# Kernel optimization log

Measured on AMD Instinct MI355X. Metric: run time of the kernel, lower is better.

## Reference

```python
import jax, jax.numpy as jnp
import numpy as np

B = 64
A_DIM, T_DIM, V_DIM = 512, 1024, 512
H = 96
O1, O2, O3 = 6, 1, 3
HP1 = H + 1  # 97


def setup_inputs() -> dict:
    key = jax.random.key(0)
    ks = jax.random.split(key, 20)
    s = 0.02
    inp = {
        "audios": jax.random.normal(ks[0], (B, A_DIM), jnp.float32),
        "texts": jax.random.normal(ks[1], (B, T_DIM), jnp.float32),
        "videos": jax.random.normal(ks[2], (B, V_DIM), jnp.float32),
        # MLP encoders: Linear(in, hidden) + ReLU (dropout is identity at eval)
        "Wa": jax.random.normal(ks[3], (A_DIM, H), jnp.float32) * s,
        "ba": jnp.zeros((H,), jnp.float32),
        "Wt": jax.random.normal(ks[4], (T_DIM, H), jnp.float32) * s,
        "bt": jnp.zeros((H,), jnp.float32),
        "Wv": jax.random.normal(ks[5], (V_DIM, H), jnp.float32) * s,
        "bv": jnp.zeros((H,), jnp.float32),
        # post-fusion MLP
        "W1": jax.random.normal(ks[6], (HP1 * HP1 * HP1, H), jnp.float32) * s,
        "b1": jnp.zeros((H,), jnp.float32),
        "W2": jax.random.normal(ks[7], (H, H), jnp.float32) * s,
        "b2": jnp.zeros((H,), jnp.float32),
        # output heads
        "Wo1": jax.random.normal(ks[8], (H, O1), jnp.float32) * s,
        "bo1": jnp.zeros((O1,), jnp.float32),
        "Wo2": jax.random.normal(ks[9], (H, O2), jnp.float32) * s,
        "bo2": jnp.zeros((O2,), jnp.float32),
        "Wo3": jax.random.normal(ks[10], (H, O3), jnp.float32) * s,
        "bo3": jnp.zeros((O3,), jnp.float32),
    }
    return inp


def reference(audios, texts, videos, Wa, ba, Wt, bt, Wv, bv,
              W1, b1, W2, b2, Wo1, bo1, Wo2, bo2, Wo3, bo3):
    # encoders (eval mode: dropout = identity)
    ah = jax.nn.relu(audios @ Wa + ba)   # [B, H]
    th = jax.nn.relu(texts @ Wt + bt)    # [B, H]
    vh = jax.nn.relu(videos @ Wv + bv)   # [B, H]

    one = jnp.ones((ah.shape[0], 1), ah.dtype)
    a1 = jnp.concatenate([one, ah], axis=1)  # [B, H+1]
    v1 = jnp.concatenate([one, vh], axis=1)  # [B, H+1]
    t1 = jnp.concatenate([one, th], axis=1)  # [B, H+1]

    # trilinear outer product: bmm(a1[:, :, None], v1[:, None, :]) -> [B, A, V]
    # then bmm with t1 -> [B, A*V, T]; flatten order is (a, v, t)
    fusion = jnp.einsum('ba,bv,bt->bavt', a1, v1, t1).reshape(a1.shape[0], -1)

    y1 = jax.nn.relu(fusion @ W1 + b1)
    features = jax.nn.relu(y1 @ W2 + b2)

    emos_out = features @ Wo1 + bo1
    vals_out = features @ Wo2 + bo2
    sents_out = features @ Wo3 + bo3
    interloss = jnp.zeros((), jnp.float32)
    return (features, emos_out, vals_out, sents_out, interloss)
```

## Files before the change

### kernel.cpp

```cpp
#include <hip/hip_runtime.h>


typedef unsigned int u32;
typedef short frag8s __attribute__((ext_vector_type(8)));
typedef float f32x4 __attribute__((ext_vector_type(4)));

constexpr int NRUN   = 9409;
constexpr int NGROUP = 2353;
constexpr int RBLK   = 776;
constexpr int NW1    = 912673 * 96;
constexpr int G3     = 512;

constexpr int WS_A1T   = 0;
constexpr int WS_V1T   = WS_A1T + 98 * 64;
constexpr int WS_T1T   = WS_V1T + 98 * 64;
constexpr int WS_Y1SUM = WS_T1T + 98 * 64;

__device__ __forceinline__ u32 bfrne(float x) {
    u32 u = __float_as_uint(x);
    return (u + 0x7FFFu + ((u >> 16) & 1u)) >> 16;
}
__device__ __forceinline__ float bflo(u32 p) { return __uint_as_float(p << 16); }
__device__ __forceinline__ float bfhi(u32 p) { return __uint_as_float(p & 0xFFFF0000u); }

__device__ __forceinline__ void async_cp16(float* lds, const float* g) {
    __builtin_amdgcn_global_load_lds((const __attribute__((address_space(1))) u32*)g,
                                     (__attribute__((address_space(3))) u32*)lds, 16, 0, 0);
}

__global__ __launch_bounds__(256) void k1_enc(const float* __restrict__ audios,
                                              const float* __restrict__ texts,
                                              const float* __restrict__ videos,
                                              const float* __restrict__ Wa, const float* __restrict__ ba,
                                              const float* __restrict__ Wt, const float* __restrict__ bt,
                                              const float* __restrict__ Wv, const float* __restrict__ bv,
                                              float* __restrict__ ws) {
    int wg = blockIdx.x, tid = threadIdx.x;
    int lane = tid & 63, wv = tid >> 6;
    if (wg == 288) {
        if (tid < 64) ws[WS_T1T + 97 * 64 + tid] = 0.0f;
        for (int i = tid; i < 6144; i += 256) ws[WS_Y1SUM + i] = 0.0f;
        return;
    }
    int e = wg / 96, h = wg % 96;
    const float* in; const float* W; float bias; int K; int outbase;
    if (e == 0)      { in = audios; W = Wa; bias = ba[h]; K = 512;  outbase = WS_A1T; }
    else if (e == 1) { in = texts;  W = Wt; bias = bt[h]; K = 1024; outbase = WS_T1T; }
    else             { in = videos; W = Wv; bias = bv[h]; K = 512;  outbase = WS_V1T; }
    int nsweep = K >> 8;
    float4 wreg[4];
    for (int s = 0; s < nsweep; s++) {
        int k0i = s * 256 + lane * 4;
        wreg[s] = make_float4(W[(k0i + 0) * 96 + h], W[(k0i + 1) * 96 + h],
                              W[(k0i + 2) * 96 + h], W[(k0i + 3) * 96 + h]);
    }
    for (int pass = 0; pass < 16; pass++) {
        int b = pass * 4 + wv;
        float acc = 0.f;
        for (int s = 0; s < nsweep; s++) {
            float4 iv = ((const float4*)(in + b * K))[s * 64 + lane];
            acc += iv.x * wreg[s].x + iv.y * wreg[s].y + iv.z * wreg[s].z + iv.w * wreg[s].w;
        }
        for (int off = 32; off; off >>= 1) acc += __shfl_down(acc, off, 64);
        if (lane == 0) {
            float v = acc + bias;
            ws[outbase + (h + 1) * 64 + b] = v > 0.f ? v : 0.f;
        }
    }
    if (h == 0 && tid < 64) ws[outbase + tid] = 1.0f;
}

__global__ __launch_bounds__(256) void k3_main(const float* __restrict__ W1,
                                               float* __restrict__ ws) {
    __shared__ float wtile[4][4 * RBLK];
    __shared__ u32   tpk[64 * 65];
    __shared__ float sl[5][256];

    int tid = threadIdx.x, lane = tid & 63, wv = tid >> 6;
    int id = blockIdx.x;
    int g0, gcount;
    if (id < 305) { g0 = id * 5;                 gcount = 5; }
    else          { g0 = 1525 + (id - 305) * 4;  gcount = 4; }
    const int L = gcount * 13;

    for (int i = tid; i < 4096; i += 256) {
        int b_ = i >> 6, p = i & 63;
        u32 v = 0;
        if (p < 49) {
            float e0 = ws[WS_T1T + (2 * p) * 64 + b_];
            float e1 = ws[WS_T1T + (2 * p + 1) * 64 + b_];
            v = bfrne(e0) | (bfrne(e1) << 16);
        }
        tpk[b_ * 65 + p] = v;
    }
    {
        int q2 = tid >> 6, b_ = tid & 63;
#pragma unroll
        for (int g2 = 0; g2 < 5; g2++) {
            float s = 0.f;
            int run = (g0 + g2) * 4 + q2;
            if (g2 < gcount && run < NRUN) {
                int i = run / 97, j = run % 97;
                s = ws[WS_A1T + i * 64 + b_] * ws[WS_V1T + j * 64 + b_];
            }
            sl[g2][tid] = s;
        }
    }

    auto stage = [&](int g, int t, int buf) {
        int idx0 = (g * 4 + wv) * (97 * 96) + t * (8 * 96) + lane * 4;
        float* ldst = &wtile[buf][wv * RBLK];
#pragma unroll
        for (int c = 0; c < 3; c++) {
            int idx = idx0 + c * 256;
            idx = idx < NW1 - 4 ? idx : NW1 - 4;
            async_cp16(ldst + c * 256, W1 + idx);
        }
    };
    int cs_g = g0, cs_t = 0;
    auto stage_next = [&](int buf) {
        stage(cs_g, cs_t, buf);
        if (++cs_t == 13) { cs_t = 0; ++cs_g; }
    };

    stage_next(0); stage_next(1); stage_next(2);
    asm volatile("s_waitcnt vmcnt(6) lgkmcnt(0)" ::: "memory");
    __builtin_amdgcn_s_barrier();

    f32x4 acc[6];
#pragma unroll
    for (int nt = 0; nt < 6; nt++) acc[nt] = f32x4{0.f, 0.f, 0.f, 0.f};

    int b = (wv << 4) + (lane & 15);
    int q = lane >> 4;

    int gi = 0, t = 0;
    for (int u = 0; u < L; ++u) {
        if (u + 3 < L) stage_next((u + 3) & 3);

        float sv = sl[gi][q * 64 + b];
        int pb = b * 65 + t * 4;
        u32 ap[4];
#pragma unroll
        for (int r = 0; r < 4; r++) {
            u32 tp = tpk[pb + r];
            float fe = sv * bflo(tp), fo = sv * bfhi(tp);
            ap[r] = bfrne(fe) | (bfrne(fo) << 16);
        }
        union { u32 u4[4]; frag8s f; } afr;
        afr.u4[0] = ap[0]; afr.u4[1] = ap[1]; afr.u4[2] = ap[2]; afr.u4[3] = ap[3];

        const float* wt0 = &wtile[u & 3][q * RBLK + (lane & 15)];
#pragma unroll
        for (int nt = 0; nt < 6; nt++) {
            union { u32 u4[4]; frag8s f; } bfr;
#pragma unroll
            for (int r = 0; r < 4; r++) {
                u32 w0 = __float_as_uint(wt0[(2 * r) * 96 + nt * 16]);
                u32 w1 = __float_as_uint(wt0[(2 * r + 1) * 96 + nt * 16]);
                bfr.u4[r] = (w0 >> 16) | (w1 & 0xFFFF0000u);
            }
            acc[nt] = __builtin_amdgcn_mfma_f32_16x16x32_bf16(afr.f, bfr.f, acc[nt], 0, 0, 0);
        }

        if (u + 4 <= L)      asm volatile("s_waitcnt vmcnt(6) lgkmcnt(0)" ::: "memory");
        else if (u + 3 == L) asm volatile("s_waitcnt vmcnt(3) lgkmcnt(0)" ::: "memory");
        else                 asm volatile("s_waitcnt vmcnt(0) lgkmcnt(0)" ::: "memory");
        __builtin_amdgcn_s_barrier();

        if (++t == 13) { t = 0; ++gi; }
    }

    float* ysum = ws + WS_Y1SUM;
#pragma unroll
    for (int nt = 0; nt < 6; nt++) {
#pragma unroll
        for (int r = 0; r < 4; r++) {
            int row = (wv << 4) + ((lane >> 4) << 2) + r;
            int col = nt * 16 + (lane & 15);
            atomicAdd(&ysum[row * 96 + col], acc[nt][r]);
        }
    }
}

__global__ __launch_bounds__(256) void k5_final(const float* __restrict__ b1,
                                                const float* __restrict__ W2, const float* __restrict__ b2,
                                                const float* __restrict__ Wo1, const float* __restrict__ bo1,
                                                const float* __restrict__ Wo2, const float* __restrict__ bo2,
                                                const float* __restrict__ Wo3, const float* __restrict__ bo3,
                                                const float* __restrict__ ws, float* __restrict__ out) {
    __shared__ float yl[8 * 96];
    __shared__ float w2l[96 * 97];
    __shared__ float fl[8 * 96];
    int tid = threadIdx.x;
    int row0 = blockIdx.x * 8;
    for (int i = tid; i < 768; i += 256) {
        int go = row0 * 96 + i;
        float acc = b1[i % 96] + ws[WS_Y1SUM + go];
        yl[i] = acc > 0.f ? acc : 0.f;
    }
    for (int i = tid; i < 9216; i += 256) { int k = i / 96, h = i % 96; w2l[k * 97 + h] = W2[i]; }
    __syncthreads();
    for (int i = tid; i < 768; i += 256) {
        int bb = i / 96, h = i % 96;
        float acc = b2[h];
#pragma unroll 8
        for (int k = 0; k < 96; k++) acc += yl[bb * 96 + k] * w2l[k * 97 + h];
        float f = acc > 0.f ? acc : 0.f;
        fl[i] = f; out[(row0 + bb) * 96 + h] = f;
    }
    __syncthreads();
    if (tid < 80) {
        if (tid < 48) {
            int lr = tid / 6, j = tid % 6;
            float acc = bo1[j];
            for (int k = 0; k < 96; k++) acc += fl[lr * 96 + k] * Wo1[k * 6 + j];
            out[6144 + (row0 + lr) * 6 + j] = acc;
        } else if (tid < 56) {
            int lr = tid - 48;
            float acc = bo2[0];
            for (int k = 0; k < 96; k++) acc += fl[lr * 96 + k] * Wo2[k];
            out[6528 + row0 + lr] = acc;
        } else {
            int t2 = tid - 56; int lr = t2 / 3, j = t2 % 3;
            float acc = bo3[j];
            for (int k = 0; k < 96; k++) acc += fl[lr * 96 + k] * Wo3[k * 3 + j];
            out[6592 + (row0 + lr) * 3 + j] = acc;
        }
    }
    if (blockIdx.x == 0 && tid == 0) out[6784] = 0.0f;
}

extern "C" void kernel_launch(void* const* d_in, const int* in_sizes, int n_in,
                              void* d_out, int out_size, void* d_ws, size_t ws_size,
                              hipStream_t stream) {
    (void)in_sizes; (void)n_in; (void)out_size; (void)ws_size;
    const float* audios = (const float*)d_in[0];
    const float* texts  = (const float*)d_in[1];
    const float* videos = (const float*)d_in[2];
    const float* Wa  = (const float*)d_in[3];
    const float* ba  = (const float*)d_in[4];
    const float* Wt  = (const float*)d_in[5];
    const float* bt  = (const float*)d_in[6];
    const float* Wv  = (const float*)d_in[7];
    const float* bv  = (const float*)d_in[8];
    const float* W1  = (const float*)d_in[9];
    const float* b1  = (const float*)d_in[10];
    const float* W2  = (const float*)d_in[11];
    const float* b2  = (const float*)d_in[12];
    const float* Wo1 = (const float*)d_in[13];
    const float* bo1 = (const float*)d_in[14];
    const float* Wo2 = (const float*)d_in[15];
    const float* bo2 = (const float*)d_in[16];
    const float* Wo3 = (const float*)d_in[17];
    const float* bo3 = (const float*)d_in[18];
    float* ws = (float*)d_ws;
    float* outp = (float*)d_out;

    k1_enc<<<289, 256, 0, stream>>>(audios, texts, videos, Wa, ba, Wt, bt, Wv, bv, ws);
    k3_main<<<G3, 256, 0, stream>>>(W1, ws);
    k5_final<<<8, 256, 0, stream>>>(b1, W2, b2, Wo1, bo1, Wo2, bo2, Wo3, bo3, ws, outp);
}
```

Measured before the change: 565.5 us.

## Replace atomic split-K reduction with per-block partials reduced in final kernel

```diff
diff --git a/kernel.cpp b/kernel.cpp
--- a/kernel.cpp
+++ b/kernel.cpp
@@ -11,10 +11,10 @@
 constexpr int NW1    = 912673 * 96;
 constexpr int G3     = 512;
 
-constexpr int WS_A1T   = 0;
-constexpr int WS_V1T   = WS_A1T + 98 * 64;
-constexpr int WS_T1T   = WS_V1T + 98 * 64;
-constexpr int WS_Y1SUM = WS_T1T + 98 * 64;
+constexpr int WS_A1T  = 0;
+constexpr int WS_V1T  = WS_A1T + 98 * 64;
+constexpr int WS_T1T  = WS_V1T + 98 * 64;
+constexpr int WS_PART = WS_T1T + 98 * 64;
 
 __device__ __forceinline__ u32 bfrne(float x) {
     u32 u = __float_as_uint(x);
@@ -39,7 +39,6 @@
     int lane = tid & 63, wv = tid >> 6;
     if (wg == 288) {
         if (tid < 64) ws[WS_T1T + 97 * 64 + tid] = 0.0f;
-        for (int i = tid; i < 6144; i += 256) ws[WS_Y1SUM + i] = 0.0f;
         return;
     }
     int e = wg / 96, h = wg % 96;
@@ -171,64 +170,73 @@
         if (++t == 13) { t = 0; ++gi; }
     }
 
-    float* ysum = ws + WS_Y1SUM;
+    float* part = ws + WS_PART + (size_t)id * 6144;
 #pragma unroll
     for (int nt = 0; nt < 6; nt++) {
 #pragma unroll
         for (int r = 0; r < 4; r++) {
             int row = (wv << 4) + ((lane >> 4) << 2) + r;
             int col = nt * 16 + (lane & 15);
-            atomicAdd(&ysum[row * 96 + col], acc[nt][r]);
-        }
-    }
-}
-
-__global__ __launch_bounds__(256) void k5_final(const float* __restrict__ b1,
+            part[row * 96 + col] = acc[nt][r];
+        }
+    }
+}
+
+__global__ __launch_bounds__(384) void k5_final(const float* __restrict__ b1,
                                                 const float* __restrict__ W2, const float* __restrict__ b2,
                                                 const float* __restrict__ Wo1, const float* __restrict__ bo1,
                                                 const float* __restrict__ Wo2, const float* __restrict__ bo2,
                                                 const float* __restrict__ Wo3, const float* __restrict__ bo3,
                                                 const float* __restrict__ ws, float* __restrict__ out) {
-    __shared__ float yl[8 * 96];
+    __shared__ float red[4][96];
+    __shared__ float yl[96];
     __shared__ float w2l[96 * 97];
-    __shared__ float fl[8 * 96];
+    __shared__ float fl[96];
     int tid = threadIdx.x;
-    int row0 = blockIdx.x * 8;
-    for (int i = tid; i < 768; i += 256) {
-        int go = row0 * 96 + i;
-        float acc = b1[i % 96] + ws[WS_Y1SUM + go];
-        yl[i] = acc > 0.f ? acc : 0.f;
-    }
-    for (int i = tid; i < 9216; i += 256) { int k = i / 96, h = i % 96; w2l[k * 97 + h] = W2[i]; }
+    int row = blockIdx.x;
+    int s = tid / 96;
+    int c = tid - s * 96;
+
+    for (int i = tid; i < 9216; i += 384) { int k = i / 96, h = i % 96; w2l[k * 97 + h] = W2[i]; }
+
+    {
+        float acc = 0.f;
+        const float* p = ws + WS_PART + (size_t)(s * 128) * 6144 + row * 96 + c;
+#pragma unroll 8
+        for (int w = 0; w < 128; w++) acc += p[(size_t)w * 6144];
+        red[s][c] = acc;
+    }
     __syncthreads();
-    for (int i = tid; i < 768; i += 256) {
-        int bb = i / 96, h = i % 96;
-        float acc = b2[h];
+    if (tid < 96) {
+        float y = red[0][tid] + red[1][tid] + red[2][tid] + red[3][tid] + b1[tid];
+        yl[tid] = y > 0.f ? y : 0.f;
+    }
+    __syncthreads();
+    if (tid < 96) {
+        float acc = b2[tid];
 #pragma unroll 8
-        for (int k = 0; k < 96; k++) acc += yl[bb * 96 + k] * w2l[k * 97 + h];
+        for (int k = 0; k < 96; k++) acc += yl[k] * w2l[k * 97 + tid];
         float f = acc > 0.f ? acc : 0.f;
-        fl[i] = f; out[(row0 + bb) * 96 + h] = f;
+        fl[tid] = f; out[row * 96 + tid] = f;
     }
     __syncthreads();
-    if (tid < 80) {
-        if (tid < 48) {
-            int lr = tid / 6, j = tid % 6;
-            float acc = bo1[j];
-            for (int k = 0; k < 96; k++) acc += fl[lr * 96 + k] * Wo1[k * 6 + j];
-            out[6144 + (row0 + lr) * 6 + j] = acc;
-        } else if (tid < 56) {
-            int lr = tid - 48;
+    if (tid < 10) {
+        if (tid < 6) {
+            float acc = bo1[tid];
+            for (int k = 0; k < 96; k++) acc += fl[k] * Wo1[k * 6 + tid];
+            out[6144 + row * 6 + tid] = acc;
+        } else if (tid == 6) {
             float acc = bo2[0];
-            for (int k = 0; k < 96; k++) acc += fl[lr * 96 + k] * Wo2[k];
-            out[6528 + row0 + lr] = acc;
+            for (int k = 0; k < 96; k++) acc += fl[k] * Wo2[k];
+            out[6528 + row] = acc;
         } else {
-            int t2 = tid - 56; int lr = t2 / 3, j = t2 % 3;
+            int j = tid - 7;
             float acc = bo3[j];
-            for (int k = 0; k < 96; k++) acc += fl[lr * 96 + k] * Wo3[k * 3 + j];
-            out[6592 + (row0 + lr) * 3 + j] = acc;
-        }
-    }
-    if (blockIdx.x == 0 && tid == 0) out[6784] = 0.0f;
+            for (int k = 0; k < 96; k++) acc += fl[k] * Wo3[k * 3 + j];
+            out[6592 + row * 3 + j] = acc;
+        }
+    }
+    if (row == 0 && tid == 0) out[6784] = 0.0f;
 }
 
 extern "C" void kernel_launch(void* const* d_in, const int* in_sizes, int n_in,
@@ -259,5 +267,5 @@
 
     k1_enc<<<289, 256, 0, stream>>>(audios, texts, videos, Wa, ba, Wt, bt, Wv, bv, ws);
     k3_main<<<G3, 256, 0, stream>>>(W1, ws);
-    k5_final<<<8, 256, 0, stream>>>(b1, W2, b2, Wo1, bo1, Wo2, bo2, Wo3, bo3, ws, outp);
-}
+    k5_final<<<64, 384, 0, stream>>>(b1, W2, b2, Wo1, bo1, Wo2, bo2, Wo3, bo3, ws, outp);
+}
```

Result: slower. 580.4 us (+2.6%).

## Transpose W1 tile into swizzled LDS layout via 4-byte async loads for vectorized B-fragment reads

Applied to the files above, without the earlier changes.

```diff
diff --git a/kernel.cpp b/kernel.cpp
--- a/kernel.cpp
+++ b/kernel.cpp
@@ -6,8 +6,6 @@
 typedef float f32x4 __attribute__((ext_vector_type(4)));
 
 constexpr int NRUN   = 9409;
-constexpr int NGROUP = 2353;
-constexpr int RBLK   = 776;
 constexpr int NW1    = 912673 * 96;
 constexpr int G3     = 512;
 
@@ -23,9 +21,9 @@
 __device__ __forceinline__ float bflo(u32 p) { return __uint_as_float(p << 16); }
 __device__ __forceinline__ float bfhi(u32 p) { return __uint_as_float(p & 0xFFFF0000u); }
 
-__device__ __forceinline__ void async_cp16(float* lds, const float* g) {
+__device__ __forceinline__ void async_cp4(float* lds, const float* g) {
     __builtin_amdgcn_global_load_lds((const __attribute__((address_space(1))) u32*)g,
-                                     (__attribute__((address_space(3))) u32*)lds, 16, 0, 0);
+                                     (__attribute__((address_space(3))) u32*)lds, 4, 0, 0);
 }
 
 __global__ __launch_bounds__(256) void k1_enc(const float* __restrict__ audios,
@@ -72,7 +70,7 @@
 
 __global__ __launch_bounds__(256) void k3_main(const float* __restrict__ W1,
                                                float* __restrict__ ws) {
-    __shared__ float wtile[4][4 * RBLK];
+    __shared__ float wtile[4][4 * 768];
     __shared__ u32   tpk[64 * 65];
     __shared__ float sl[5][256];
 
@@ -107,14 +105,23 @@
         }
     }
 
+    int goff[12];
+#pragma unroll
+    for (int c = 0; c < 12; c++) {
+        int S = c * 64 + lane;
+        int col = S >> 3;
+        int j = (S & 7) ^ (((S >> 5) & 1) << 2);
+        goff[c] = j * 96 + col;
+    }
+
     auto stage = [&](int g, int t, int buf) {
-        int idx0 = (g * 4 + wv) * (97 * 96) + t * (8 * 96) + lane * 4;
-        float* ldst = &wtile[buf][wv * RBLK];
-#pragma unroll
-        for (int c = 0; c < 3; c++) {
-            int idx = idx0 + c * 256;
-            idx = idx < NW1 - 4 ? idx : NW1 - 4;
-            async_cp16(ldst + c * 256, W1 + idx);
+        int runbase = (g * 4 + wv) * (97 * 96) + t * (8 * 96);
+        float* ldst = &wtile[buf][wv * 768];
+#pragma unroll
+        for (int c = 0; c < 12; c++) {
+            int idx = runbase + goff[c];
+            idx = idx < NW1 - 1 ? idx : NW1 - 1;
+            async_cp4(ldst + c * 64, W1 + idx);
         }
     };
     int cs_g = g0, cs_t = 0;
@@ -124,15 +131,19 @@
     };
 
     stage_next(0); stage_next(1); stage_next(2);
-    asm volatile("s_waitcnt vmcnt(6) lgkmcnt(0)" ::: "memory");
+    asm volatile("s_waitcnt vmcnt(24) lgkmcnt(0)" ::: "memory");
     __builtin_amdgcn_s_barrier();
 
     f32x4 acc[6];
 #pragma unroll
     for (int nt = 0; nt < 6; nt++) acc[nt] = f32x4{0.f, 0.f, 0.f, 0.f};
 
-    int b = (wv << 4) + (lane & 15);
+    int c16 = lane & 15;
+    int b = (wv << 4) + c16;
     int q = lane >> 4;
+    int f = (c16 >> 2) & 1;
+    int blo = q * 768 + c16 * 8 + 4 * f;
+    int bhi = q * 768 + c16 * 8 + 4 * (1 - f);
 
     int gi = 0, t = 0;
     for (int u = 0; u < L; ++u) {
@@ -147,24 +158,24 @@
             float fe = sv * bflo(tp), fo = sv * bfhi(tp);
             ap[r] = bfrne(fe) | (bfrne(fo) << 16);
         }
-        union { u32 u4[4]; frag8s f; } afr;
+        union { u32 u4[4]; frag8s f8; } afr;
         afr.u4[0] = ap[0]; afr.u4[1] = ap[1]; afr.u4[2] = ap[2]; afr.u4[3] = ap[3];
 
-        const float* wt0 = &wtile[u & 3][q * RBLK + (lane & 15)];
+        const float* wb = wtile[u & 3];
 #pragma unroll
         for (int nt = 0; nt < 6; nt++) {
-            union { u32 u4[4]; frag8s f; } bfr;
-#pragma unroll
-            for (int r = 0; r < 4; r++) {
-                u32 w0 = __float_as_uint(wt0[(2 * r) * 96 + nt * 16]);
-                u32 w1 = __float_as_uint(wt0[(2 * r + 1) * 96 + nt * 16]);
-                bfr.u4[r] = (w0 >> 16) | (w1 & 0xFFFF0000u);
-            }
-            acc[nt] = __builtin_amdgcn_mfma_f32_16x16x32_bf16(afr.f, bfr.f, acc[nt], 0, 0, 0);
-        }
-
-        if (u + 4 <= L)      asm volatile("s_waitcnt vmcnt(6) lgkmcnt(0)" ::: "memory");
-        else if (u + 3 == L) asm volatile("s_waitcnt vmcnt(3) lgkmcnt(0)" ::: "memory");
+            f32x4 lo = *(const f32x4*)(wb + blo + nt * 128);
+            f32x4 hi = *(const f32x4*)(wb + bhi + nt * 128);
+            union { u32 u4[4]; frag8s f8; } bfr;
+            bfr.u4[0] = __builtin_amdgcn_perm(__float_as_uint(lo[1]), __float_as_uint(lo[0]), 0x07060302u);
+            bfr.u4[1] = __builtin_amdgcn_perm(__float_as_uint(lo[3]), __float_as_uint(lo[2]), 0x07060302u);
+            bfr.u4[2] = __builtin_amdgcn_perm(__float_as_uint(hi[1]), __float_as_uint(hi[0]), 0x07060302u);
+            bfr.u4[3] = __builtin_amdgcn_perm(__float_as_uint(hi[3]), __float_as_uint(hi[2]), 0x07060302u);
+            acc[nt] = __builtin_amdgcn_mfma_f32_16x16x32_bf16(afr.f8, bfr.f8, acc[nt], 0, 0, 0);
+        }
+
+        if (u + 4 <= L)      asm volatile("s_waitcnt vmcnt(24) lgkmcnt(0)" ::: "memory");
+        else if (u + 3 == L) asm volatile("s_waitcnt vmcnt(12) lgkmcnt(0)" ::: "memory");
         else                 asm volatile("s_waitcnt vmcnt(0) lgkmcnt(0)" ::: "memory");
         __builtin_amdgcn_s_barrier();
 
```

New measurement: 576.0 us. No clear change (+1.9%).
